# Kernel tuning notes

Hardware: AMD Instinct MI355X
Metric: run time of the kernel (lower is better)

Reference implementation:

```python
import jax, jax.numpy as jnp
import numpy as np

B, N, D = 16, 4096, 128

def setup_inputs() -> dict:
    key = jax.random.key(0)
    ks = jax.random.split(key, 6)
    return {
        "x": jax.random.normal(ks[0], (B, N), dtype=jnp.float32),
        "q_w": jax.random.normal(ks[1], (D,), dtype=jnp.float32) * 0.1,
        "q_b": jax.random.normal(ks[2], (D,), dtype=jnp.float32) * 0.1,
        "k_w": jax.random.normal(ks[3], (D,), dtype=jnp.float32) * 0.1,
        "k_b": jax.random.normal(ks[4], (D,), dtype=jnp.float32) * 0.1,
        "pos_embed": jax.random.normal(ks[5], (N, D), dtype=jnp.float32) * 0.1,
    }

def reference(x, q_w, q_b, k_w, k_b, pos_embed):
    # x: [B, N]. Linear(1, D) on x.unsqueeze(-1) == outer-product broadcast.
    n = x.shape[1]
    pe = pos_embed[:n]                                   # [N, D]
    q = x[:, :, None] * q_w + q_b + pe                   # [B, N, D]
    k = x[:, :, None] * k_w + k_b + pe                   # [B, N, D]
    scale = 1.0 / jnp.sqrt(jnp.asarray(q.shape[-1], q.dtype))
    scores = jnp.einsum("bid,bjd->bij", q, k) * scale    # [B, N, N]
    attn = jax.nn.softmax(scores, axis=-1)
    # value is x.unsqueeze(-1): head-dim 1 -> contract directly with x
    out = jnp.einsum("bij,bj->bi", attn, x)              # [B, N]
    return out
```

## Files before the change

kernel.cpp:

```cpp
#include <hip/hip_runtime.h>
#include <cstdint>

#define NN 4096
#define DD 128
#define NB 16
#define JSPLIT 8
#define JRANGE (NN / JSPLIT)
#define WJ (JRANGE / 4)
#define NCH (WJ / 16)

typedef __attribute__((ext_vector_type(8))) short short8;
typedef __attribute__((ext_vector_type(4))) float f32x4;
typedef unsigned short u16;

#define S2 (0.088388347648318447f * 1.4426950408889634f)

__device__ __forceinline__ u16 f2bf(float f) {
  union { float f; unsigned int u; } v; v.f = f;
  unsigned int u = v.u;
  u += 0x7fffu + ((u >> 16) & 1u);
  return (u16)(u >> 16);
}

__global__ void precomp_kernel(const float* __restrict__ q_w, const float* __restrict__ q_b,
                               const float* __restrict__ k_w, const float* __restrict__ k_b,
                               const float* __restrict__ pe,
                               u16* __restrict__ Qbh, u16* __restrict__ Kbh,
                               float* __restrict__ A2, float* __restrict__ B2,
                               float* __restrict__ c2p) {
  const int t = threadIdx.x, lane = t & 63, wv = t >> 6;
  const int row = blockIdx.x * 4 + wv;

  const float p0 = pe[row * DD + lane];
  const float p1 = pe[row * DD + 64 + lane];
  const float qv0 = q_b[lane] + p0, qv1 = q_b[lane + 64] + p1;
  const float kv0 = k_b[lane] + p0, kv1 = k_b[lane + 64] + p1;
  const float qw0 = q_w[lane], qw1 = q_w[lane + 64];
  const float kw0 = k_w[lane], kw1 = k_w[lane + 64];

  Qbh[row * DD + lane]      = f2bf(qv0 * S2);
  Qbh[row * DD + 64 + lane] = f2bf(qv1 * S2);
  Kbh[row * DD + lane]      = f2bf(kv0);
  Kbh[row * DD + 64 + lane] = f2bf(kv1);

  float asum = qw0 * kv0 + qw1 * kv1;
  float bsum = kw0 * qv0 + kw1 * qv1;
#pragma unroll
  for (int m = 1; m < 64; m <<= 1) {
    asum += __shfl_xor(asum, m);
    bsum += __shfl_xor(bsum, m);
  }
  if (lane == 0) { A2[row] = S2 * asum; B2[row] = S2 * bsum; }

  if (row == 0) {
    float csum = qw0 * kw0 + qw1 * kw1;
#pragma unroll
    for (int m = 1; m < 64; m <<= 1) csum += __shfl_xor(csum, m);
    if (lane == 0) *c2p = S2 * csum;
  }
}

__global__ __launch_bounds__(256, 4) void attn_main(
    const float* __restrict__ x, const u16* __restrict__ Qbh,
    const u16* __restrict__ Kbh, const float* __restrict__ A2,
    const float* __restrict__ B2, const float* __restrict__ c2p,
    float* __restrict__ part_l, float* __restrict__ part_o) {
  __shared__ __align__(16) float smem[16 * 512 + 512];

  const int t = threadIdx.x;
  const int lane = t & 63, w = t >> 6;
  const int il = lane & 15, h = lane >> 4;
  const int i0 = blockIdx.x * 16;
  const int js = blockIdx.y;
  const int jb = js * JRANGE;

  const float c2 = *c2p;
  const float B2i = B2[i0 + il];

#pragma unroll
  for (int it = 0; it < 8; ++it) {
    const int flat = it * 256 + t;
    const int b = flat >> 7, c4 = flat & 127;
    *(float4*)(&smem[b * 512 + c4 * 4]) =
        *(const float4*)(x + b * NN + jb + c4 * 4);
  }
  if (t < 128)
    *(float4*)(&smem[8192 + t * 4]) = *(const float4*)(A2 + jb + t * 4);

  short8 qfr[4];
#pragma unroll
  for (int ks = 0; ks < 4; ++ks)
    qfr[ks] = *(const short8*)(Qbh + (i0 + il) * DD + ks * 32 + h * 8);

  float xi[16];
#pragma unroll
  for (int b = 0; b < 16; ++b) xi[b] = x[b * NN + i0 + il];

  float l[16], o[16];
#pragma unroll
  for (int b = 0; b < 16; ++b) { l[b] = 0.f; o[b] = 0.f; }

  __syncthreads();

  const float* xw  = &smem[w * WJ + 4 * h];
  const float* a2w = &smem[8192 + w * WJ + 4 * h];
  const u16*   kb  = Kbh + (jb + w * WJ + il) * DD + h * 8;

  short8 kfr[4];
#pragma unroll
  for (int ks = 0; ks < 4; ++ks) kfr[ks] = *(const short8*)(kb + ks * 32);

  for (int c = 0; c < NCH; ++c) {
    f32x4 acc = {0.f, 0.f, 0.f, 0.f};
#pragma unroll
    for (int ks = 0; ks < 4; ++ks)
      acc = __builtin_amdgcn_mfma_f32_16x16x32_bf16(kfr[ks], qfr[ks], acc, 0, 0, 0);

    if (c + 1 < NCH) {
      const u16* kbn = kb + (c + 1) * 16 * DD;
#pragma unroll
      for (int ks = 0; ks < 4; ++ks) kfr[ks] = *(const short8*)(kbn + ks * 32);
    }

    const float4 a2c = *(const float4*)(a2w + c * 16);
    const float* xc = xw + c * 16;

#pragma unroll
    for (int b = 0; b < 16; ++b) {
      const float4 xv = *(const float4*)(xc + b * 512);
      const float Vb = fmaf(c2, xi[b], B2i);
      const float t0 = fmaf(xi[b], a2c.x, acc[0]);
      const float t1 = fmaf(xi[b], a2c.y, acc[1]);
      const float t2 = fmaf(xi[b], a2c.z, acc[2]);
      const float t3 = fmaf(xi[b], a2c.w, acc[3]);
      const float s0 = fmaf(xv.x, Vb, t0);
      const float s1 = fmaf(xv.y, Vb, t1);
      const float s2 = fmaf(xv.z, Vb, t2);
      const float s3 = fmaf(xv.w, Vb, t3);
      const float e0 = __builtin_amdgcn_exp2f(s0);
      const float e1 = __builtin_amdgcn_exp2f(s1);
      const float e2 = __builtin_amdgcn_exp2f(s2);
      const float e3 = __builtin_amdgcn_exp2f(s3);
      l[b] += (e0 + e1) + (e2 + e3);
      float ob = o[b];
      ob = fmaf(e0, xv.x, ob);
      ob = fmaf(e1, xv.y, ob);
      ob = fmaf(e2, xv.z, ob);
      ob = fmaf(e3, xv.w, ob);
      o[b] = ob;
    }
  }

  __syncthreads();
#pragma unroll
  for (int b = 0; b < 16; ++b) {
    float lv = l[b], ov = o[b];
    lv += __shfl_xor(lv, 16); lv += __shfl_xor(lv, 32);
    ov += __shfl_xor(ov, 16); ov += __shfl_xor(ov, 32);
    if (h == 0) {
      smem[(w * 16 + b) * 16 + il]        = lv;
      smem[4096 + (w * 16 + b) * 16 + il] = ov;
    }
  }
  __syncthreads();

  {
    const int b = t >> 4, ii = t & 15;
    float lsum = 0.f, osum = 0.f;
#pragma unroll
    for (int ww = 0; ww < 4; ++ww) {
      lsum += smem[(ww * 16 + b) * 16 + ii];
      osum += smem[4096 + (ww * 16 + b) * 16 + ii];
    }
    const int outidx = (js * NB + b) * NN + i0 + ii;
    part_l[outidx] = lsum;
    part_o[outidx] = osum;
  }
}

__global__ void combine_kernel(const float* __restrict__ part_l,
                               const float* __restrict__ part_o,
                               float* __restrict__ out) {
  const int id = blockIdx.x * 256 + threadIdx.x;
  float l = 0.f, o = 0.f;
#pragma unroll
  for (int js = 0; js < JSPLIT; ++js) {
    l += part_l[js * (NB * NN) + id];
    o += part_o[js * (NB * NN) + id];
  }
  out[id] = o / l;
}

extern "C" void kernel_launch(void* const* d_in, const int* in_sizes, int n_in,
                              void* d_out, int out_size, void* d_ws, size_t ws_size,
                              hipStream_t stream) {
  const float* x   = (const float*)d_in[0];
  const float* q_w = (const float*)d_in[1];
  const float* q_b = (const float*)d_in[2];
  const float* k_w = (const float*)d_in[3];
  const float* k_b = (const float*)d_in[4];
  const float* pe  = (const float*)d_in[5];
  float* out = (float*)d_out;

  char* ws = (char*)d_ws;
  u16*   Qbh    = (u16*)(ws);
  u16*   Kbh    = (u16*)(ws + (1u << 20));
  float* A2     = (float*)(ws + (2u << 20));
  float* B2     = (float*)(ws + (2u << 20) + (16u << 10));
  float* c2p    = (float*)(ws + (2u << 20) + (32u << 10));
  float* part_l = (float*)(ws + (2u << 20) + (48u << 10));
  float* part_o = (float*)(ws + (2u << 20) + (48u << 10) + (2u << 20));

  precomp_kernel<<<NN / 4, 256, 0, stream>>>(q_w, q_b, k_w, k_b, pe,
                                             Qbh, Kbh, A2, B2, c2p);
  attn_main<<<dim3(NN / 16, JSPLIT), 256, 0, stream>>>(x, Qbh, Kbh, A2, B2, c2p,
                                                       part_l, part_o);
  combine_kernel<<<(NB * NN) / 256, 256, 0, stream>>>(part_l, part_o, out);
}
```

Before: 67.67 us.

## Restructure attention into 256-column segments with larger j-split and packed FMAs

```diff
diff --git a/kernel.cpp b/kernel.cpp
--- a/kernel.cpp
+++ b/kernel.cpp
@@ -4,16 +4,21 @@
 #define NN 4096
 #define DD 128
 #define NB 16
-#define JSPLIT 8
-#define JRANGE (NN / JSPLIT)
-#define WJ (JRANGE / 4)
-#define NCH (WJ / 16)
 
 typedef __attribute__((ext_vector_type(8))) short short8;
 typedef __attribute__((ext_vector_type(4))) float f32x4;
+typedef __attribute__((ext_vector_type(2))) float f32x2;
 typedef unsigned short u16;
 
 #define S2 (0.088388347648318447f * 1.4426950408889634f)
+
+static __device__ __forceinline__ f32x2 pkfma(f32x2 a, f32x2 b, f32x2 c) {
+#if __has_builtin(__builtin_elementwise_fma)
+  return __builtin_elementwise_fma(a, b, c);
+#else
+  return a * b + c;
+#endif
+}
 
 __device__ __forceinline__ u16 f2bf(float f) {
   union { float f; unsigned int u; } v; v.f = f;
@@ -60,12 +65,18 @@
   }
 }
 
-__global__ __launch_bounds__(256, 4) void attn_main(
+template <int JSPLIT>
+__global__ __launch_bounds__(256, 5) void attn_main(
     const float* __restrict__ x, const u16* __restrict__ Qbh,
     const u16* __restrict__ Kbh, const float* __restrict__ A2,
     const float* __restrict__ B2, const float* __restrict__ c2p,
     float* __restrict__ part_l, float* __restrict__ part_o) {
-  __shared__ __align__(16) float smem[16 * 512 + 512];
+  constexpr int JRANGE = NN / JSPLIT;
+  constexpr int NSEG = JRANGE / 256;
+
+  __shared__ __align__(16) float xs[16 * 256];
+  __shared__ __align__(16) float a2s[256];
+  __shared__ __align__(16) float red[2048];
 
   const int t = threadIdx.x;
   const int lane = t & 63, w = t >> 6;
@@ -77,100 +88,97 @@
   const float c2 = *c2p;
   const float B2i = B2[i0 + il];
 
-#pragma unroll
-  for (int it = 0; it < 8; ++it) {
-    const int flat = it * 256 + t;
-    const int b = flat >> 7, c4 = flat & 127;
-    *(float4*)(&smem[b * 512 + c4 * 4]) =
-        *(const float4*)(x + b * NN + jb + c4 * 4);
-  }
-  if (t < 128)
-    *(float4*)(&smem[8192 + t * 4]) = *(const float4*)(A2 + jb + t * 4);
-
   short8 qfr[4];
 #pragma unroll
   for (int ks = 0; ks < 4; ++ks)
     qfr[ks] = *(const short8*)(Qbh + (i0 + il) * DD + ks * 32 + h * 8);
 
-  float xi[16];
-#pragma unroll
-  for (int b = 0; b < 16; ++b) xi[b] = x[b * NN + i0 + il];
-
-  float l[16], o[16];
-#pragma unroll
-  for (int b = 0; b < 16; ++b) { l[b] = 0.f; o[b] = 0.f; }
+  for (int seg = 0; seg < NSEG; ++seg) {
+    const int j0 = jb + seg * 256;
+    __syncthreads();
+#pragma unroll
+    for (int it = 0; it < 4; ++it) {
+      const int flat = it * 256 + t;
+      const int b = flat >> 6, c4 = flat & 63;
+      *(float4*)(&xs[b * 256 + c4 * 4]) =
+          *(const float4*)(x + b * NN + j0 + c4 * 4);
+    }
+    if (t < 64)
+      *(float4*)(&a2s[t * 4]) = *(const float4*)(A2 + j0 + t * 4);
+    __syncthreads();
+
+    f32x4 acc[4];
+    {
+      const u16* kb = Kbh + (j0 + w * 64 + il) * DD + h * 8;
+#pragma unroll
+      for (int c = 0; c < 4; ++c) {
+        short8 kfr[4];
+#pragma unroll
+        for (int ks = 0; ks < 4; ++ks)
+          kfr[ks] = *(const short8*)(kb + c * 16 * DD + ks * 32);
+        f32x4 a = {0.f, 0.f, 0.f, 0.f};
+#pragma unroll
+        for (int ks = 0; ks < 4; ++ks)
+          a = __builtin_amdgcn_mfma_f32_16x16x32_bf16(kfr[ks], qfr[ks], a, 0, 0, 0);
+        acc[c] = a;
+      }
+    }
+
+    float4 a2v[4];
+#pragma unroll
+    for (int c = 0; c < 4; ++c)
+      a2v[c] = *(const float4*)(&a2s[w * 64 + c * 16 + 4 * h]);
+
+    const float* xw = &xs[w * 64 + 4 * h];
+
+    float xic = x[i0 + il];
+#pragma unroll
+    for (int b = 0; b < 16; ++b) {
+      float xin = 0.f;
+      if (b < 15) xin = x[(b + 1) * NN + i0 + il];
+      const f32x2 xib = {xic, xic};
+      const float Vb = fmaf(c2, xic, B2i);
+      const f32x2 Vb2 = {Vb, Vb};
+      f32x2 l2 = {0.f, 0.f}, o2 = {0.f, 0.f};
+#pragma unroll
+      for (int c = 0; c < 4; ++c) {
+        const float4 xv = *(const float4*)(xw + b * 256 + c * 16);
+        const f32x2 xv01 = {xv.x, xv.y}, xv23 = {xv.z, xv.w};
+        const f32x2 alo = {a2v[c].x, a2v[c].y}, ahi = {a2v[c].z, a2v[c].w};
+        const f32x2 clo = {acc[c][0], acc[c][1]}, chi = {acc[c][2], acc[c][3]};
+        const f32x2 s01 = pkfma(xv01, Vb2, pkfma(xib, alo, clo));
+        const f32x2 s23 = pkfma(xv23, Vb2, pkfma(xib, ahi, chi));
+        const f32x2 e01 = {__builtin_amdgcn_exp2f(s01[0]),
+                           __builtin_amdgcn_exp2f(s01[1])};
+        const f32x2 e23 = {__builtin_amdgcn_exp2f(s23[0]),
+                           __builtin_amdgcn_exp2f(s23[1])};
+        l2 += e01; l2 += e23;
+        o2 = pkfma(e01, xv01, o2);
+        o2 = pkfma(e23, xv23, o2);
+      }
+      float lv = l2[0] + l2[1], ov = o2[0] + o2[1];
+      lv += __shfl_xor(lv, 16); lv += __shfl_xor(lv, 32);
+      ov += __shfl_xor(ov, 16); ov += __shfl_xor(ov, 32);
+      if (h == 0) {
+        const int ri = (w * 16 + b) * 16 + il;
+        if (NSEG == 1 || seg == 0) {
+          red[ri] = lv; red[1024 + ri] = ov;
+        } else {
+          red[ri] += lv; red[1024 + ri] += ov;
+        }
+      }
+      xic = xin;
+    }
+  }
 
   __syncthreads();
-
-  const float* xw  = &smem[w * WJ + 4 * h];
-  const float* a2w = &smem[8192 + w * WJ + 4 * h];
-  const u16*   kb  = Kbh + (jb + w * WJ + il) * DD + h * 8;
-
-  short8 kfr[4];
-#pragma unroll
-  for (int ks = 0; ks < 4; ++ks) kfr[ks] = *(const short8*)(kb + ks * 32);
-
-  for (int c = 0; c < NCH; ++c) {
-    f32x4 acc = {0.f, 0.f, 0.f, 0.f};
-#pragma unroll
-    for (int ks = 0; ks < 4; ++ks)
-      acc = __builtin_amdgcn_mfma_f32_16x16x32_bf16(kfr[ks], qfr[ks], acc, 0, 0, 0);
-
-    if (c + 1 < NCH) {
-      const u16* kbn = kb + (c + 1) * 16 * DD;
-#pragma unroll
-      for (int ks = 0; ks < 4; ++ks) kfr[ks] = *(const short8*)(kbn + ks * 32);
-    }
-
-    const float4 a2c = *(const float4*)(a2w + c * 16);
-    const float* xc = xw + c * 16;
-
-#pragma unroll
-    for (int b = 0; b < 16; ++b) {
-      const float4 xv = *(const float4*)(xc + b * 512);
-      const float Vb = fmaf(c2, xi[b], B2i);
-      const float t0 = fmaf(xi[b], a2c.x, acc[0]);
-      const float t1 = fmaf(xi[b], a2c.y, acc[1]);
-      const float t2 = fmaf(xi[b], a2c.z, acc[2]);
-      const float t3 = fmaf(xi[b], a2c.w, acc[3]);
-      const float s0 = fmaf(xv.x, Vb, t0);
-      const float s1 = fmaf(xv.y, Vb, t1);
-      const float s2 = fmaf(xv.z, Vb, t2);
-      const float s3 = fmaf(xv.w, Vb, t3);
-      const float e0 = __builtin_amdgcn_exp2f(s0);
-      const float e1 = __builtin_amdgcn_exp2f(s1);
-      const float e2 = __builtin_amdgcn_exp2f(s2);
-      const float e3 = __builtin_amdgcn_exp2f(s3);
-      l[b] += (e0 + e1) + (e2 + e3);
-      float ob = o[b];
-      ob = fmaf(e0, xv.x, ob);
-      ob = fmaf(e1, xv.y, ob);
-      ob = fmaf(e2, xv.z, ob);
-      ob = fmaf(e3, xv.w, ob);
-      o[b] = ob;
-    }
-  }
-
-  __syncthreads();
-#pragma unroll
-  for (int b = 0; b < 16; ++b) {
-    float lv = l[b], ov = o[b];
-    lv += __shfl_xor(lv, 16); lv += __shfl_xor(lv, 32);
-    ov += __shfl_xor(ov, 16); ov += __shfl_xor(ov, 32);
-    if (h == 0) {
-      smem[(w * 16 + b) * 16 + il]        = lv;
-      smem[4096 + (w * 16 + b) * 16 + il] = ov;
-    }
-  }
-  __syncthreads();
-
   {
     const int b = t >> 4, ii = t & 15;
     float lsum = 0.f, osum = 0.f;
 #pragma unroll
     for (int ww = 0; ww < 4; ++ww) {
-      lsum += smem[(ww * 16 + b) * 16 + ii];
-      osum += smem[4096 + (ww * 16 + b) * 16 + ii];
+      lsum += red[(ww * 16 + b) * 16 + ii];
+      osum += red[1024 + (ww * 16 + b) * 16 + ii];
     }
     const int outidx = (js * NB + b) * NN + i0 + ii;
     part_l[outidx] = lsum;
@@ -178,6 +186,7 @@
   }
 }
 
+template <int JSPLIT>
 __global__ void combine_kernel(const float* __restrict__ part_l,
                                const float* __restrict__ part_o,
                                float* __restrict__ out) {
@@ -209,11 +218,21 @@
   float* B2     = (float*)(ws + (2u << 20) + (16u << 10));
   float* c2p    = (float*)(ws + (2u << 20) + (32u << 10));
   float* part_l = (float*)(ws + (2u << 20) + (48u << 10));
-  float* part_o = (float*)(ws + (2u << 20) + (48u << 10) + (2u << 20));
 
   precomp_kernel<<<NN / 4, 256, 0, stream>>>(q_w, q_b, k_w, k_b, pe,
                                              Qbh, Kbh, A2, B2, c2p);
-  attn_main<<<dim3(NN / 16, JSPLIT), 256, 0, stream>>>(x, Qbh, Kbh, A2, B2, c2p,
-                                                       part_l, part_o);
-  combine_kernel<<<(NB * NN) / 256, 256, 0, stream>>>(part_l, part_o, out);
-}
+
+  const size_t base = (size_t)(2u << 20) + (48u << 10);
+  const size_t need16 = base + 2 * (size_t)16 * NB * NN * 4;
+  if (ws_size >= need16) {
+    float* part_o = (float*)(ws + base + (size_t)16 * NB * NN * 4);
+    attn_main<16><<<dim3(NN / 16, 16), 256, 0, stream>>>(
+        x, Qbh, Kbh, A2, B2, c2p, part_l, part_o);
+    combine_kernel<16><<<(NB * NN) / 256, 256, 0, stream>>>(part_l, part_o, out);
+  } else {
+    float* part_o = (float*)(ws + base + (size_t)8 * NB * NN * 4);
+    attn_main<8><<<dim3(NN / 16, 8), 256, 0, stream>>>(
+        x, Qbh, Kbh, A2, B2, c2p, part_l, part_o);
+    combine_kernel<8><<<(NB * NN) / 256, 256, 0, stream>>>(part_l, part_o, out);
+  }
+}
```

After: 69.78 us. 1.03x slower.
